# Kernel optimization log

Hardware: AMD Instinct MI355X
Metric: run time of the kernel (lower is better)

Reference implementation:

```python
import jax, jax.numpy as jnp
import numpy as np

N_NODES = 100000
N_EDGES = 1600000
DIM = 64
LAYERS = 2


def setup_inputs() -> dict:
    key = jax.random.key(0)
    k1, k2, k3, k4 = jax.random.split(key, 4)
    h = jax.random.normal(k1, (N_NODES, DIM), dtype=jnp.float32)
    w = jax.random.uniform(k2, (N_EDGES,), dtype=jnp.float32)
    src = jax.random.randint(k3, (N_EDGES,), 0, N_NODES, dtype=jnp.int32)
    dst = jax.random.randint(k4, (N_EDGES,), 0, N_NODES, dtype=jnp.int32)
    return {"h": h, "w": w, "src": src, "dst": dst}


def reference(h, w, src, dst):
    N = h.shape[0]
    # weighted in-degree, clamped at 1 (DGL in_degrees(weight='w').clamp(min=1))
    deg = jnp.maximum(jax.ops.segment_sum(w, dst, num_segments=N), 1.0)
    norm = deg[:, None] ** -0.5  # [N, 1]
    embs = [h]
    for _ in range(LAYERS):
        h_norm = h * norm                              # [N, d]
        m = h_norm[src] * w[:, None]                   # [E, d] edge messages (u_mul_e)
        neigh_sum = jax.ops.segment_sum(m, dst, num_segments=N)  # fn.sum
        h = neigh_sum * norm
        embs.append(h)
    # mean over [h0, h1, ..., hL]
    return jnp.mean(jnp.stack(embs, axis=1), axis=1)
```

## Files before the change

### kernel.cpp

```cpp
#include <hip/hip_runtime.h>
#include <hip/hip_bf16.h>

#define D 64
#define THREADS 256
#define BKT_BITS 9
#define BKT_NODES (1 << BKT_BITS)
#define CHUNK 8192

__device__ __forceinline__ unsigned f2bf(float f) {
    unsigned u = __float_as_uint(f);
    return (u + 0x7fffu + ((u >> 16) & 1u)) >> 16;
}
__device__ __forceinline__ float2 bfpair(unsigned v) {
    return make_float2(__uint_as_float(v << 16), __uint_as_float(v & 0xffff0000u));
}

__global__ void p1a_hist(const int* __restrict__ dst, int* __restrict__ blockCount,
                         int E, int B) {
    __shared__ int lc[256];
    int t = threadIdx.x;
    lc[t] = 0;
    __syncthreads();
    int base = blockIdx.x * CHUNK;
    int end = min(base + CHUNK, E);
    for (int e = base + t; e < end; e += THREADS)
        atomicAdd(&lc[dst[e] >> BKT_BITS], 1);
    __syncthreads();
    if (t < B) blockCount[(long long)blockIdx.x * B + t] = lc[t];
}

__global__ void p1b_scanblocks(int* __restrict__ blockCount, int* __restrict__ total,
                               int NBLK, int B) {
    __shared__ int sm[256];
    int b = blockIdx.x, t = threadIdx.x;
    int run = 0;
    for (int base = 0; base < NBLK; base += 256) {
        int i = base + t;
        int v = (i < NBLK) ? blockCount[(long long)i * B + b] : 0;
        sm[t] = v;
        __syncthreads();
        for (int off = 1; off < 256; off <<= 1) {
            int u = (t >= off) ? sm[t - off] : 0;
            __syncthreads();
            sm[t] += u;
            __syncthreads();
        }
        if (i < NBLK) blockCount[(long long)i * B + b] = run + sm[t] - v;
        run += sm[255];
        __syncthreads();
    }
    if (t == 0) total[b] = run;
}

__global__ void p1c_scanbuckets(const int* __restrict__ total, int* __restrict__ bstart,
                                int B, int E) {
    __shared__ int sm[256];
    int t = threadIdx.x;
    int run = 0;
    for (int base = 0; base < B; base += 256) {
        int i = base + t;
        int v = (i < B) ? total[i] : 0;
        sm[t] = v;
        __syncthreads();
        for (int off = 1; off < 256; off <<= 1) {
            int u = (t >= off) ? sm[t - off] : 0;
            __syncthreads();
            sm[t] += u;
            __syncthreads();
        }
        if (i < B) bstart[i] = run + sm[t] - v;
        run += sm[255];
        __syncthreads();
    }
    if (t == 0) bstart[B] = E;
}

__global__ void p1d_scatter(const int* __restrict__ dst, const int* __restrict__ src,
                            const float* __restrict__ w, const int* __restrict__ blockCount,
                            const int* __restrict__ bstart, int2* __restrict__ temp,
                            int E, int B) {
    __shared__ int cur[256];
    int t = threadIdx.x;
    if (t < B) cur[t] = bstart[t] + blockCount[(long long)blockIdx.x * B + t];
    __syncthreads();
    int base = blockIdx.x * CHUNK;
    int end = min(base + CHUNK, E);
    for (int e = base + t; e < end; e += THREADS) {
        int d = dst[e];
        int b = d >> BKT_BITS;
        int pos = atomicAdd(&cur[b], 1);
        temp[pos] = make_int2(src[e] | ((d & (BKT_NODES - 1)) << 17),
                              __float_as_int(w[e]));
    }
}

__global__ void p2a_build(const int2* __restrict__ temp, const int* __restrict__ bstart,
                          int* __restrict__ rowptr, float* __restrict__ norm,
                          int N, int E, int B) {
    __shared__ int cnt[BKT_NODES];
    __shared__ float degs[BKT_NODES];
    __shared__ int sm[256];
    int b = blockIdx.x, t = threadIdx.x;
    int ebeg = bstart[b], eend = bstart[b + 1];
    for (int i = t; i < BKT_NODES; i += THREADS) { cnt[i] = 0; degs[i] = 0.0f; }
    __syncthreads();
    for (int e = ebeg + t; e < eend; e += THREADS) {
        int2 pk = temp[e];
        int dl = (pk.x >> 17) & (BKT_NODES - 1);
        atomicAdd(&cnt[dl], 1);
        atomicAdd(&degs[dl], __int_as_float(pk.y));
    }
    __syncthreads();
    int node0 = b << BKT_BITS;
    int run = 0;
    for (int base = 0; base < BKT_NODES; base += 256) {
        int v = cnt[base + t];
        sm[t] = v;
        __syncthreads();
        for (int off = 1; off < 256; off <<= 1) {
            int u = (t >= off) ? sm[t - off] : 0;
            __syncthreads();
            sm[t] += u;
            __syncthreads();
        }
        int node = node0 + base + t;
        if (node < N) {
            rowptr[node] = ebeg + run + sm[t] - v;
            norm[node] = rsqrtf(fmaxf(degs[base + t], 1.0f));
        }
        run += sm[255];
        __syncthreads();
    }
    if (b == 0 && t == 0) rowptr[N] = E;
}

__global__ void p2b_place(const int2* __restrict__ temp, const int* __restrict__ bstart,
                          const int* __restrict__ rowptr, const float* __restrict__ norm,
                          int2* __restrict__ packed, int N, int E) {
    __shared__ int cur[BKT_NODES];
    int b = blockIdx.x, t = threadIdx.x;
    int ebeg = bstart[b], eend = bstart[b + 1];
    int node0 = b << BKT_BITS;
    for (int i = t; i < BKT_NODES; i += THREADS) {
        int node = node0 + i;
        cur[i] = (node < N) ? (rowptr[node] - ebeg) : 0;
    }
    __syncthreads();
    for (int e = ebeg + t; e < eend; e += THREADS) {
        int2 pk = temp[e];
        int dl = (pk.x >> 17) & (BKT_NODES - 1);
        int s = pk.x & 0x1ffff;
        float coef = __int_as_float(pk.y) * norm[s];
        int pos = atomicAdd(&cur[dl], 1);
        packed[ebeg + pos] = make_int2(s, __float_as_int(coef));
    }
}

__global__ void tobf16_kernel(const float* __restrict__ h, unsigned* __restrict__ hbf2,
                              long long nd4) {
    long long i = (long long)blockIdx.x * blockDim.x + threadIdx.x;
    if (i < nd4) {
        float4 v = ((const float4*)h)[i];
        ((uint2*)hbf2)[i] = make_uint2(f2bf(v.x) | (f2bf(v.y) << 16),
                                       f2bf(v.z) | (f2bf(v.w) << 16));
    }
}

#define EDGE_FMA(r, c, A0, A1, A2, A3, A4, A5, A6, A7) do {            \
    float2 fa = bfpair((r).x), fb = bfpair((r).y);                      \
    float2 fc = bfpair((r).z), fd = bfpair((r).w);                      \
    A0 = fmaf(fa.x, (c), A0); A1 = fmaf(fa.y, (c), A1);                 \
    A2 = fmaf(fb.x, (c), A2); A3 = fmaf(fb.y, (c), A3);                 \
    A4 = fmaf(fc.x, (c), A4); A5 = fmaf(fc.y, (c), A5);                 \
    A6 = fmaf(fd.x, (c), A6); A7 = fmaf(fd.y, (c), A7); } while (0)

__global__ void gather1_kernel(const uint4* __restrict__ h_in, const int2* __restrict__ packed,
                               const int* __restrict__ rowptr, const float* __restrict__ norm,
                               uint4* __restrict__ h_out, int N) {
    int node = blockIdx.x * (blockDim.x >> 3) + (threadIdx.x >> 3);
    int lane = threadIdx.x & 7;
    if (node >= N) return;
    int j = rowptr[node], end = rowptr[node + 1];
    float a0 = 0, a1 = 0, a2 = 0, a3 = 0, a4 = 0, a5 = 0, a6 = 0, a7 = 0;
    float b0 = 0, b1 = 0, b2 = 0, b3 = 0, b4 = 0, b5 = 0, b6 = 0, b7 = 0;
    for (; j + 8 <= end; j += 8) {
        int2 p0 = packed[j + 0], p1 = packed[j + 1], p2 = packed[j + 2], p3 = packed[j + 3];
        int2 p4 = packed[j + 4], p5 = packed[j + 5], p6 = packed[j + 6], p7 = packed[j + 7];
        uint4 r0 = h_in[((long long)p0.x << 3) + lane];
        uint4 r1 = h_in[((long long)p1.x << 3) + lane];
        uint4 r2 = h_in[((long long)p2.x << 3) + lane];
        uint4 r3 = h_in[((long long)p3.x << 3) + lane];
        uint4 r4 = h_in[((long long)p4.x << 3) + lane];
        uint4 r5 = h_in[((long long)p5.x << 3) + lane];
        uint4 r6 = h_in[((long long)p6.x << 3) + lane];
        uint4 r7 = h_in[((long long)p7.x << 3) + lane];
        EDGE_FMA(r0, __int_as_float(p0.y), a0, a1, a2, a3, a4, a5, a6, a7);
        EDGE_FMA(r1, __int_as_float(p1.y), b0, b1, b2, b3, b4, b5, b6, b7);
        EDGE_FMA(r2, __int_as_float(p2.y), a0, a1, a2, a3, a4, a5, a6, a7);
        EDGE_FMA(r3, __int_as_float(p3.y), b0, b1, b2, b3, b4, b5, b6, b7);
        EDGE_FMA(r4, __int_as_float(p4.y), a0, a1, a2, a3, a4, a5, a6, a7);
        EDGE_FMA(r5, __int_as_float(p5.y), b0, b1, b2, b3, b4, b5, b6, b7);
        EDGE_FMA(r6, __int_as_float(p6.y), a0, a1, a2, a3, a4, a5, a6, a7);
        EDGE_FMA(r7, __int_as_float(p7.y), b0, b1, b2, b3, b4, b5, b6, b7);
    }
    for (; j + 4 <= end; j += 4) {
        int2 p0 = packed[j + 0], p1 = packed[j + 1], p2 = packed[j + 2], p3 = packed[j + 3];
        uint4 r0 = h_in[((long long)p0.x << 3) + lane];
        uint4 r1 = h_in[((long long)p1.x << 3) + lane];
        uint4 r2 = h_in[((long long)p2.x << 3) + lane];
        uint4 r3 = h_in[((long long)p3.x << 3) + lane];
        EDGE_FMA(r0, __int_as_float(p0.y), a0, a1, a2, a3, a4, a5, a6, a7);
        EDGE_FMA(r1, __int_as_float(p1.y), b0, b1, b2, b3, b4, b5, b6, b7);
        EDGE_FMA(r2, __int_as_float(p2.y), a0, a1, a2, a3, a4, a5, a6, a7);
        EDGE_FMA(r3, __int_as_float(p3.y), b0, b1, b2, b3, b4, b5, b6, b7);
    }
    for (; j < end; ++j) {
        int2 p = packed[j];
        uint4 r = h_in[((long long)p.x << 3) + lane];
        EDGE_FMA(r, __int_as_float(p.y), a0, a1, a2, a3, a4, a5, a6, a7);
    }
    float nv = norm[node];
    float d0 = (a0 + b0) * nv, d1 = (a1 + b1) * nv, d2 = (a2 + b2) * nv, d3 = (a3 + b3) * nv;
    float d4 = (a4 + b4) * nv, d5 = (a5 + b5) * nv, d6 = (a6 + b6) * nv, d7 = (a7 + b7) * nv;
    h_out[((long long)node << 3) + lane] =
        make_uint4(f2bf(d0) | (f2bf(d1) << 16), f2bf(d2) | (f2bf(d3) << 16),
                   f2bf(d4) | (f2bf(d5) << 16), f2bf(d6) | (f2bf(d7) << 16));
}

__global__ void gather2_final_kernel(const uint4* __restrict__ h0bf, const uint4* __restrict__ h1bf,
                                     const int2* __restrict__ packed, const int* __restrict__ rowptr,
                                     const float* __restrict__ norm, float* __restrict__ out, int N) {
    int node = blockIdx.x * (blockDim.x >> 3) + (threadIdx.x >> 3);
    int lane = threadIdx.x & 7;
    if (node >= N) return;
    int j = rowptr[node], end = rowptr[node + 1];
    float a0 = 0, a1 = 0, a2 = 0, a3 = 0, a4 = 0, a5 = 0, a6 = 0, a7 = 0;
    float b0 = 0, b1 = 0, b2 = 0, b3 = 0, b4 = 0, b5 = 0, b6 = 0, b7 = 0;
    for (; j + 8 <= end; j += 8) {
        int2 p0 = packed[j + 0], p1 = packed[j + 1], p2 = packed[j + 2], p3 = packed[j + 3];
        int2 p4 = packed[j + 4], p5 = packed[j + 5], p6 = packed[j + 6], p7 = packed[j + 7];
        uint4 r0 = h1bf[((long long)p0.x << 3) + lane];
        uint4 r1 = h1bf[((long long)p1.x << 3) + lane];
        uint4 r2 = h1bf[((long long)p2.x << 3) + lane];
        uint4 r3 = h1bf[((long long)p3.x << 3) + lane];
        uint4 r4 = h1bf[((long long)p4.x << 3) + lane];
        uint4 r5 = h1bf[((long long)p5.x << 3) + lane];
        uint4 r6 = h1bf[((long long)p6.x << 3) + lane];
        uint4 r7 = h1bf[((long long)p7.x << 3) + lane];
        EDGE_FMA(r0, __int_as_float(p0.y), a0, a1, a2, a3, a4, a5, a6, a7);
        EDGE_FMA(r1, __int_as_float(p1.y), b0, b1, b2, b3, b4, b5, b6, b7);
        EDGE_FMA(r2, __int_as_float(p2.y), a0, a1, a2, a3, a4, a5, a6, a7);
        EDGE_FMA(r3, __int_as_float(p3.y), b0, b1, b2, b3, b4, b5, b6, b7);
        EDGE_FMA(r4, __int_as_float(p4.y), a0, a1, a2, a3, a4, a5, a6, a7);
        EDGE_FMA(r5, __int_as_float(p5.y), b0, b1, b2, b3, b4, b5, b6, b7);
        EDGE_FMA(r6, __int_as_float(p6.y), a0, a1, a2, a3, a4, a5, a6, a7);
        EDGE_FMA(r7, __int_as_float(p7.y), b0, b1, b2, b3, b4, b5, b6, b7);
    }
    for (; j + 4 <= end; j += 4) {
        int2 p0 = packed[j + 0], p1 = packed[j + 1], p2 = packed[j + 2], p3 = packed[j + 3];
        uint4 r0 = h1bf[((long long)p0.x << 3) + lane];
        uint4 r1 = h1bf[((long long)p1.x << 3) + lane];
        uint4 r2 = h1bf[((long long)p2.x << 3) + lane];
        uint4 r3 = h1bf[((long long)p3.x << 3) + lane];
        EDGE_FMA(r0, __int_as_float(p0.y), a0, a1, a2, a3, a4, a5, a6, a7);
        EDGE_FMA(r1, __int_as_float(p1.y), b0, b1, b2, b3, b4, b5, b6, b7);
        EDGE_FMA(r2, __int_as_float(p2.y), a0, a1, a2, a3, a4, a5, a6, a7);
        EDGE_FMA(r3, __int_as_float(p3.y), b0, b1, b2, b3, b4, b5, b6, b7);
    }
    for (; j < end; ++j) {
        int2 p = packed[j];
        uint4 r = h1bf[((long long)p.x << 3) + lane];
        EDGE_FMA(r, __int_as_float(p.y), a0, a1, a2, a3, a4, a5, a6, a7);
    }
    long long idx = ((long long)node << 3) + lane;
    float nv = norm[node];
    uint4 h0r = h0bf[idx], h1r = h1bf[idx];
    float2 h0a = bfpair(h0r.x), h0b = bfpair(h0r.y), h0c = bfpair(h0r.z), h0d = bfpair(h0r.w);
    float2 h1a = bfpair(h1r.x), h1b = bfpair(h1r.y), h1c = bfpair(h1r.z), h1d = bfpair(h1r.w);
    float4 o0, o1;
    o0.x = (h0a.x + h1a.x + (a0 + b0) * nv) * (1.0f / 3.0f);
    o0.y = (h0a.y + h1a.y + (a1 + b1) * nv) * (1.0f / 3.0f);
    o0.z = (h0b.x + h1b.x + (a2 + b2) * nv) * (1.0f / 3.0f);
    o0.w = (h0b.y + h1b.y + (a3 + b3) * nv) * (1.0f / 3.0f);
    o1.x = (h0c.x + h1c.x + (a4 + b4) * nv) * (1.0f / 3.0f);
    o1.y = (h0c.y + h1c.y + (a5 + b5) * nv) * (1.0f / 3.0f);
    o1.z = (h0d.x + h1d.x + (a6 + b6) * nv) * (1.0f / 3.0f);
    o1.w = (h0d.y + h1d.y + (a7 + b7) * nv) * (1.0f / 3.0f);
    ((float4*)out)[((long long)node << 4) + (lane << 1)] = o0;
    ((float4*)out)[((long long)node << 4) + (lane << 1) + 1] = o1;
}

extern "C" void kernel_launch(void* const* d_in, const int* in_sizes, int n_in,
                              void* d_out, int out_size, void* d_ws, size_t ws_size,
                              hipStream_t stream) {
    const float* h   = (const float*)d_in[0];
    const float* w   = (const float*)d_in[1];
    const int*   src = (const int*)d_in[2];
    const int*   dst = (const int*)d_in[3];
    const int N = in_sizes[0] / D;
    const int E = in_sizes[1];
    float* out = (float*)d_out;

    const int B = (N + BKT_NODES - 1) >> BKT_BITS;
    const int NBLK = (E + CHUNK - 1) / CHUNK;

    char* ws = (char*)d_ws;
    size_t off = 0;
    auto alloc = [&](size_t bytes, size_t align) -> char* {
        off = (off + align - 1) & ~(align - 1);
        char* p = ws + off;
        off += bytes;
        return p;
    };
    float* norm     = (float*)alloc((size_t)N * 4, 16);
    int*   rowptr   = (int*)  alloc((size_t)(N + 1) * 4, 16);
    int*   total    = (int*)  alloc((size_t)B * 4, 16);
    int*   bstart   = (int*)  alloc((size_t)(B + 1) * 4, 16);
    int*   blockCnt = (int*)  alloc((size_t)NBLK * B * 4, 16);
    int2*  packed   = (int2*) alloc((size_t)E * 8, 16);
    char*  shared_region = alloc((size_t)E * 8, 128);
    int2*     temp = (int2*)shared_region;
    unsigned* h1bf = (unsigned*)shared_region;
    unsigned* h0bf = (unsigned*)alloc((size_t)N * D * 2, 128);

    const int nodes_per_block = THREADS / 8;
    const int gather_blocks = (N + nodes_per_block - 1) / nodes_per_block;
    const long long nd4 = (long long)N * D / 4;
    const int cvt_blocks = (int)((nd4 + THREADS - 1) / THREADS);

    p1a_hist<<<NBLK, THREADS, 0, stream>>>(dst, blockCnt, E, B);
    p1b_scanblocks<<<B, 256, 0, stream>>>(blockCnt, total, NBLK, B);
    p1c_scanbuckets<<<1, 256, 0, stream>>>(total, bstart, B, E);
    p1d_scatter<<<NBLK, THREADS, 0, stream>>>(dst, src, w, blockCnt, bstart, temp, E, B);
    p2a_build<<<B, 256, 0, stream>>>(temp, bstart, rowptr, norm, N, E, B);
    p2b_place<<<B, 256, 0, stream>>>(temp, bstart, rowptr, norm, packed, N, E);

    tobf16_kernel<<<cvt_blocks, THREADS, 0, stream>>>(h, h0bf, nd4);

    gather1_kernel<<<gather_blocks, THREADS, 0, stream>>>((const uint4*)h0bf, packed, rowptr,
                                                          norm, (uint4*)h1bf, N);
    gather2_final_kernel<<<gather_blocks, THREADS, 0, stream>>>((const uint4*)h0bf, (const uint4*)h1bf,
                                                                packed, rowptr, norm, out, N);
}
```

Measured before the change: 230.7 us.

## Replace two-pass bucketed CSR build with global-atomic counting sort; add nontemporal loads/stores

Replaces the bucket histogram, block scan, temp scatter and per-bucket place pipeline with a simpler CSR build. Per-node counts and weighted degrees are accumulated with global atomics, scanned per bucket, and edges are placed with a global atomic cursor per node. This removes the intermediate temp array and one full pass over the edges, but relies on contended global atomics with scattered writes, and edge order within a row becomes nondeterministic. The gather kernels now use nontemporal loads for edge records and h0, and nontemporal stores for outputs, to reduce cache pollution.

```diff
diff --git a/kernel.cpp b/kernel.cpp
--- a/kernel.cpp
+++ b/kernel.cpp
@@ -5,7 +5,6 @@
 #define THREADS 256
 #define BKT_BITS 9
 #define BKT_NODES (1 << BKT_BITS)
-#define CHUNK 8192
 
 __device__ __forceinline__ unsigned f2bf(float f) {
     unsigned u = __float_as_uint(f);
@@ -15,44 +14,54 @@
     return make_float2(__uint_as_float(v << 16), __uint_as_float(v & 0xffff0000u));
 }
 
-__global__ void p1a_hist(const int* __restrict__ dst, int* __restrict__ blockCount,
-                         int E, int B) {
-    __shared__ int lc[256];
-    int t = threadIdx.x;
-    lc[t] = 0;
-    __syncthreads();
-    int base = blockIdx.x * CHUNK;
-    int end = min(base + CHUNK, E);
-    for (int e = base + t; e < end; e += THREADS)
-        atomicAdd(&lc[dst[e] >> BKT_BITS], 1);
-    __syncthreads();
-    if (t < B) blockCount[(long long)blockIdx.x * B + t] = lc[t];
-}
-
-__global__ void p1b_scanblocks(int* __restrict__ blockCount, int* __restrict__ total,
-                               int NBLK, int B) {
+typedef unsigned long long u64t;
+typedef float f32x4 __attribute__((ext_vector_type(4)));
+typedef unsigned u32x4 __attribute__((ext_vector_type(4)));
+
+__device__ __forceinline__ int2 ldnt_int2(const int2* p) {
+    u64t v = __builtin_nontemporal_load((const u64t*)p);
+    int2 r;
+    r.x = (int)(unsigned)(v & 0xffffffffull);
+    r.y = (int)(unsigned)(v >> 32);
+    return r;
+}
+__device__ __forceinline__ uint4 ldnt_uint4(const uint4* p) {
+    u32x4 v = __builtin_nontemporal_load((const u32x4*)p);
+    return make_uint4(v.x, v.y, v.z, v.w);
+}
+__device__ __forceinline__ void stnt_f4(float4 v, float4* p) {
+    f32x4 t = {v.x, v.y, v.z, v.w};
+    __builtin_nontemporal_store(t, (f32x4*)p);
+}
+__device__ __forceinline__ void stnt_u4(uint4 v, uint4* p) {
+    u32x4 t = {v.x, v.y, v.z, v.w};
+    __builtin_nontemporal_store(t, (u32x4*)p);
+}
+
+__global__ void deg_kernel(const int* __restrict__ dst, const float* __restrict__ w,
+                           int* __restrict__ cnt, float* __restrict__ degf, int E) {
+    int e = blockIdx.x * blockDim.x + threadIdx.x;
+    if (e < E) {
+        int d = dst[e];
+        atomicAdd(&cnt[d], 1);
+        atomicAdd(&degf[d], w[e]);
+    }
+}
+
+__global__ void b2a_sum(const int* __restrict__ cnt, int* __restrict__ total) {
     __shared__ int sm[256];
     int b = blockIdx.x, t = threadIdx.x;
-    int run = 0;
-    for (int base = 0; base < NBLK; base += 256) {
-        int i = base + t;
-        int v = (i < NBLK) ? blockCount[(long long)i * B + b] : 0;
-        sm[t] = v;
-        __syncthreads();
-        for (int off = 1; off < 256; off <<= 1) {
-            int u = (t >= off) ? sm[t - off] : 0;
-            __syncthreads();
-            sm[t] += u;
-            __syncthreads();
-        }
-        if (i < NBLK) blockCount[(long long)i * B + b] = run + sm[t] - v;
-        run += sm[255];
-        __syncthreads();
-    }
-    if (t == 0) total[b] = run;
-}
-
-__global__ void p1c_scanbuckets(const int* __restrict__ total, int* __restrict__ bstart,
+    int base = b << BKT_BITS;
+    sm[t] = cnt[base + t] + cnt[base + 256 + t];
+    __syncthreads();
+    for (int off = 128; off > 0; off >>= 1) {
+        if (t < off) sm[t] += sm[t + off];
+        __syncthreads();
+    }
+    if (t == 0) total[b] = sm[0];
+}
+
+__global__ void b2b_scanbuckets(const int* __restrict__ total, int* __restrict__ bstart,
                                 int B, int E) {
     __shared__ int sm[256];
     int t = threadIdx.x;
@@ -75,46 +84,15 @@
     if (t == 0) bstart[B] = E;
 }
 
-__global__ void p1d_scatter(const int* __restrict__ dst, const int* __restrict__ src,
-                            const float* __restrict__ w, const int* __restrict__ blockCount,
-                            const int* __restrict__ bstart, int2* __restrict__ temp,
-                            int E, int B) {
-    __shared__ int cur[256];
-    int t = threadIdx.x;
-    if (t < B) cur[t] = bstart[t] + blockCount[(long long)blockIdx.x * B + t];
-    __syncthreads();
-    int base = blockIdx.x * CHUNK;
-    int end = min(base + CHUNK, E);
-    for (int e = base + t; e < end; e += THREADS) {
-        int d = dst[e];
-        int b = d >> BKT_BITS;
-        int pos = atomicAdd(&cur[b], 1);
-        temp[pos] = make_int2(src[e] | ((d & (BKT_NODES - 1)) << 17),
-                              __float_as_int(w[e]));
-    }
-}
-
-__global__ void p2a_build(const int2* __restrict__ temp, const int* __restrict__ bstart,
-                          int* __restrict__ rowptr, float* __restrict__ norm,
-                          int N, int E, int B) {
-    __shared__ int cnt[BKT_NODES];
-    __shared__ float degs[BKT_NODES];
+__global__ void b2c_scan(const int* __restrict__ cnt, const float* __restrict__ degf,
+                         const int* __restrict__ bstart, int* __restrict__ rowptr,
+                         int* __restrict__ gcur, float* __restrict__ norm, int N, int E) {
     __shared__ int sm[256];
     int b = blockIdx.x, t = threadIdx.x;
-    int ebeg = bstart[b], eend = bstart[b + 1];
-    for (int i = t; i < BKT_NODES; i += THREADS) { cnt[i] = 0; degs[i] = 0.0f; }
-    __syncthreads();
-    for (int e = ebeg + t; e < eend; e += THREADS) {
-        int2 pk = temp[e];
-        int dl = (pk.x >> 17) & (BKT_NODES - 1);
-        atomicAdd(&cnt[dl], 1);
-        atomicAdd(&degs[dl], __int_as_float(pk.y));
-    }
-    __syncthreads();
-    int node0 = b << BKT_BITS;
-    int run = 0;
+    int run = bstart[b];
     for (int base = 0; base < BKT_NODES; base += 256) {
-        int v = cnt[base + t];
+        int i = (b << BKT_BITS) + base + t;
+        int v = cnt[i];
         sm[t] = v;
         __syncthreads();
         for (int off = 1; off < 256; off <<= 1) {
@@ -123,10 +101,11 @@
             sm[t] += u;
             __syncthreads();
         }
-        int node = node0 + base + t;
-        if (node < N) {
-            rowptr[node] = ebeg + run + sm[t] - v;
-            norm[node] = rsqrtf(fmaxf(degs[base + t], 1.0f));
+        int ex = run + sm[t] - v;
+        if (i < N) {
+            rowptr[i] = ex;
+            gcur[i] = ex;
+            norm[i] = rsqrtf(fmaxf(degf[i], 1.0f));
         }
         run += sm[255];
         __syncthreads();
@@ -134,25 +113,15 @@
     if (b == 0 && t == 0) rowptr[N] = E;
 }
 
-__global__ void p2b_place(const int2* __restrict__ temp, const int* __restrict__ bstart,
-                          const int* __restrict__ rowptr, const float* __restrict__ norm,
-                          int2* __restrict__ packed, int N, int E) {
-    __shared__ int cur[BKT_NODES];
-    int b = blockIdx.x, t = threadIdx.x;
-    int ebeg = bstart[b], eend = bstart[b + 1];
-    int node0 = b << BKT_BITS;
-    for (int i = t; i < BKT_NODES; i += THREADS) {
-        int node = node0 + i;
-        cur[i] = (node < N) ? (rowptr[node] - ebeg) : 0;
-    }
-    __syncthreads();
-    for (int e = ebeg + t; e < eend; e += THREADS) {
-        int2 pk = temp[e];
-        int dl = (pk.x >> 17) & (BKT_NODES - 1);
-        int s = pk.x & 0x1ffff;
-        float coef = __int_as_float(pk.y) * norm[s];
-        int pos = atomicAdd(&cur[dl], 1);
-        packed[ebeg + pos] = make_int2(s, __float_as_int(coef));
+__global__ void scatter_kernel(const int* __restrict__ dst, const int* __restrict__ src,
+                               const float* __restrict__ w, const float* __restrict__ norm,
+                               int* __restrict__ gcur, int2* __restrict__ packed, int E) {
+    int e = blockIdx.x * blockDim.x + threadIdx.x;
+    if (e < E) {
+        int d = dst[e], s = src[e];
+        float coef = w[e] * norm[s];
+        int pos = atomicAdd(&gcur[d], 1);
+        packed[pos] = make_int2(s, __float_as_int(coef));
     }
 }
 
@@ -184,8 +153,10 @@
     float a0 = 0, a1 = 0, a2 = 0, a3 = 0, a4 = 0, a5 = 0, a6 = 0, a7 = 0;
     float b0 = 0, b1 = 0, b2 = 0, b3 = 0, b4 = 0, b5 = 0, b6 = 0, b7 = 0;
     for (; j + 8 <= end; j += 8) {
-        int2 p0 = packed[j + 0], p1 = packed[j + 1], p2 = packed[j + 2], p3 = packed[j + 3];
-        int2 p4 = packed[j + 4], p5 = packed[j + 5], p6 = packed[j + 6], p7 = packed[j + 7];
+        int2 p0 = ldnt_int2(&packed[j + 0]), p1 = ldnt_int2(&packed[j + 1]);
+        int2 p2 = ldnt_int2(&packed[j + 2]), p3 = ldnt_int2(&packed[j + 3]);
+        int2 p4 = ldnt_int2(&packed[j + 4]), p5 = ldnt_int2(&packed[j + 5]);
+        int2 p6 = ldnt_int2(&packed[j + 6]), p7 = ldnt_int2(&packed[j + 7]);
         uint4 r0 = h_in[((long long)p0.x << 3) + lane];
         uint4 r1 = h_in[((long long)p1.x << 3) + lane];
         uint4 r2 = h_in[((long long)p2.x << 3) + lane];
@@ -204,7 +175,8 @@
         EDGE_FMA(r7, __int_as_float(p7.y), b0, b1, b2, b3, b4, b5, b6, b7);
     }
     for (; j + 4 <= end; j += 4) {
-        int2 p0 = packed[j + 0], p1 = packed[j + 1], p2 = packed[j + 2], p3 = packed[j + 3];
+        int2 p0 = ldnt_int2(&packed[j + 0]), p1 = ldnt_int2(&packed[j + 1]);
+        int2 p2 = ldnt_int2(&packed[j + 2]), p3 = ldnt_int2(&packed[j + 3]);
         uint4 r0 = h_in[((long long)p0.x << 3) + lane];
         uint4 r1 = h_in[((long long)p1.x << 3) + lane];
         uint4 r2 = h_in[((long long)p2.x << 3) + lane];
@@ -215,16 +187,16 @@
         EDGE_FMA(r3, __int_as_float(p3.y), b0, b1, b2, b3, b4, b5, b6, b7);
     }
     for (; j < end; ++j) {
-        int2 p = packed[j];
+        int2 p = ldnt_int2(&packed[j]);
         uint4 r = h_in[((long long)p.x << 3) + lane];
         EDGE_FMA(r, __int_as_float(p.y), a0, a1, a2, a3, a4, a5, a6, a7);
     }
     float nv = norm[node];
     float d0 = (a0 + b0) * nv, d1 = (a1 + b1) * nv, d2 = (a2 + b2) * nv, d3 = (a3 + b3) * nv;
     float d4 = (a4 + b4) * nv, d5 = (a5 + b5) * nv, d6 = (a6 + b6) * nv, d7 = (a7 + b7) * nv;
-    h_out[((long long)node << 3) + lane] =
-        make_uint4(f2bf(d0) | (f2bf(d1) << 16), f2bf(d2) | (f2bf(d3) << 16),
-                   f2bf(d4) | (f2bf(d5) << 16), f2bf(d6) | (f2bf(d7) << 16));
+    stnt_u4(make_uint4(f2bf(d0) | (f2bf(d1) << 16), f2bf(d2) | (f2bf(d3) << 16),
+                       f2bf(d4) | (f2bf(d5) << 16), f2bf(d6) | (f2bf(d7) << 16)),
+            &h_out[((long long)node << 3) + lane]);
 }
 
 __global__ void gather2_final_kernel(const uint4* __restrict__ h0bf, const uint4* __restrict__ h1bf,
@@ -237,8 +209,10 @@
     float a0 = 0, a1 = 0, a2 = 0, a3 = 0, a4 = 0, a5 = 0, a6 = 0, a7 = 0;
     float b0 = 0, b1 = 0, b2 = 0, b3 = 0, b4 = 0, b5 = 0, b6 = 0, b7 = 0;
     for (; j + 8 <= end; j += 8) {
-        int2 p0 = packed[j + 0], p1 = packed[j + 1], p2 = packed[j + 2], p3 = packed[j + 3];
-        int2 p4 = packed[j + 4], p5 = packed[j + 5], p6 = packed[j + 6], p7 = packed[j + 7];
+        int2 p0 = ldnt_int2(&packed[j + 0]), p1 = ldnt_int2(&packed[j + 1]);
+        int2 p2 = ldnt_int2(&packed[j + 2]), p3 = ldnt_int2(&packed[j + 3]);
+        int2 p4 = ldnt_int2(&packed[j + 4]), p5 = ldnt_int2(&packed[j + 5]);
+        int2 p6 = ldnt_int2(&packed[j + 6]), p7 = ldnt_int2(&packed[j + 7]);
         uint4 r0 = h1bf[((long long)p0.x << 3) + lane];
         uint4 r1 = h1bf[((long long)p1.x << 3) + lane];
         uint4 r2 = h1bf[((long long)p2.x << 3) + lane];
@@ -257,7 +231,8 @@
         EDGE_FMA(r7, __int_as_float(p7.y), b0, b1, b2, b3, b4, b5, b6, b7);
     }
     for (; j + 4 <= end; j += 4) {
-        int2 p0 = packed[j + 0], p1 = packed[j + 1], p2 = packed[j + 2], p3 = packed[j + 3];
+        int2 p0 = ldnt_int2(&packed[j + 0]), p1 = ldnt_int2(&packed[j + 1]);
+        int2 p2 = ldnt_int2(&packed[j + 2]), p3 = ldnt_int2(&packed[j + 3]);
         uint4 r0 = h1bf[((long long)p0.x << 3) + lane];
         uint4 r1 = h1bf[((long long)p1.x << 3) + lane];
         uint4 r2 = h1bf[((long long)p2.x << 3) + lane];
@@ -268,13 +243,14 @@
         EDGE_FMA(r3, __int_as_float(p3.y), b0, b1, b2, b3, b4, b5, b6, b7);
     }
     for (; j < end; ++j) {
-        int2 p = packed[j];
+        int2 p = ldnt_int2(&packed[j]);
         uint4 r = h1bf[((long long)p.x << 3) + lane];
         EDGE_FMA(r, __int_as_float(p.y), a0, a1, a2, a3, a4, a5, a6, a7);
     }
     long long idx = ((long long)node << 3) + lane;
     float nv = norm[node];
-    uint4 h0r = h0bf[idx], h1r = h1bf[idx];
+    uint4 h0r = ldnt_uint4(&h0bf[idx]);
+    uint4 h1r = h1bf[idx];
     float2 h0a = bfpair(h0r.x), h0b = bfpair(h0r.y), h0c = bfpair(h0r.z), h0d = bfpair(h0r.w);
     float2 h1a = bfpair(h1r.x), h1b = bfpair(h1r.y), h1c = bfpair(h1r.z), h1d = bfpair(h1r.w);
     float4 o0, o1;
@@ -286,8 +262,8 @@
     o1.y = (h0c.y + h1c.y + (a5 + b5) * nv) * (1.0f / 3.0f);
     o1.z = (h0d.x + h1d.x + (a6 + b6) * nv) * (1.0f / 3.0f);
     o1.w = (h0d.y + h1d.y + (a7 + b7) * nv) * (1.0f / 3.0f);
-    ((float4*)out)[((long long)node << 4) + (lane << 1)] = o0;
-    ((float4*)out)[((long long)node << 4) + (lane << 1) + 1] = o1;
+    stnt_f4(o0, &((float4*)out)[((long long)node << 4) + (lane << 1)]);
+    stnt_f4(o1, &((float4*)out)[((long long)node << 4) + (lane << 1) + 1]);
 }
 
 extern "C" void kernel_launch(void* const* d_in, const int* in_sizes, int n_in,
@@ -302,7 +278,7 @@
     float* out = (float*)d_out;
 
     const int B = (N + BKT_NODES - 1) >> BKT_BITS;
-    const int NBLK = (E + CHUNK - 1) / CHUNK;
+    const int NPAD = B << BKT_BITS;
 
     char* ws = (char*)d_ws;
     size_t off = 0;
@@ -316,24 +292,25 @@
     int*   rowptr   = (int*)  alloc((size_t)(N + 1) * 4, 16);
     int*   total    = (int*)  alloc((size_t)B * 4, 16);
     int*   bstart   = (int*)  alloc((size_t)(B + 1) * 4, 16);
-    int*   blockCnt = (int*)  alloc((size_t)NBLK * B * 4, 16);
-    int2*  packed   = (int2*) alloc((size_t)E * 8, 16);
-    char*  shared_region = alloc((size_t)E * 8, 128);
-    int2*     temp = (int2*)shared_region;
-    unsigned* h1bf = (unsigned*)shared_region;
-    unsigned* h0bf = (unsigned*)alloc((size_t)N * D * 2, 128);
+    int*   gcur     = (int*)  alloc((size_t)N * 4, 16);
+    int*   cnt      = (int*)  alloc((size_t)NPAD * 8, 16);
+    float* degf     = (float*)(cnt + NPAD);
+    int2*  packed   = (int2*) alloc((size_t)E * 8, 128);
+    unsigned* h1bf  = (unsigned*)alloc((size_t)N * D * 2, 128);
+    unsigned* h0bf  = (unsigned*)alloc((size_t)N * D * 2, 128);
 
     const int nodes_per_block = THREADS / 8;
     const int gather_blocks = (N + nodes_per_block - 1) / nodes_per_block;
     const long long nd4 = (long long)N * D / 4;
     const int cvt_blocks = (int)((nd4 + THREADS - 1) / THREADS);
-
-    p1a_hist<<<NBLK, THREADS, 0, stream>>>(dst, blockCnt, E, B);
-    p1b_scanblocks<<<B, 256, 0, stream>>>(blockCnt, total, NBLK, B);
-    p1c_scanbuckets<<<1, 256, 0, stream>>>(total, bstart, B, E);
-    p1d_scatter<<<NBLK, THREADS, 0, stream>>>(dst, src, w, blockCnt, bstart, temp, E, B);
-    p2a_build<<<B, 256, 0, stream>>>(temp, bstart, rowptr, norm, N, E, B);
-    p2b_place<<<B, 256, 0, stream>>>(temp, bstart, rowptr, norm, packed, N, E);
+    const int edge_blocks = (E + THREADS - 1) / THREADS;
+
+    hipMemsetAsync(cnt, 0, (size_t)NPAD * 8, stream);
+    deg_kernel<<<edge_blocks, THREADS, 0, stream>>>(dst, w, cnt, degf, E);
+    b2a_sum<<<B, 256, 0, stream>>>(cnt, total);
+    b2b_scanbuckets<<<1, 256, 0, stream>>>(total, bstart, B, E);
+    b2c_scan<<<B, 256, 0, stream>>>(cnt, degf, bstart, rowptr, gcur, norm, N, E);
+    scatter_kernel<<<edge_blocks, THREADS, 0, stream>>>(dst, src, w, norm, gcur, packed, E);
 
     tobf16_kernel<<<cvt_blocks, THREADS, 0, stream>>>(h, h0bf, nd4);
 
```

Result: slower. 413.5 us (+79.2%).
